# Kernel optimization log

Measured on AMD Instinct MI355X. Metric: run time of the kernel, lower is better.

Reference implementation:

```python
import jax, jax.numpy as jnp
import numpy as np

BETA = 1.0
GAMMA = 1.0
TAU = 1.0
EPS = 1e-8
RANK_CLAMP = 10  # torch.clamp(rank, max=10)


def _pearson(a, b):
    # a, b: [N, D]; pearson correlation along axis 1
    a = a - a.mean(axis=1, keepdims=True)
    b = b - b.mean(axis=1, keepdims=True)
    num = (a * b).sum(axis=1)
    den = jnp.linalg.norm(a, axis=1) * jnp.linalg.norm(b, axis=1) + EPS
    return num / den


def _filtered_ranks(y):
    # Vectorized equivalent of the per-row python loop: for each row, drop the
    # rank entry at the argmax position, yielding [B, C-1].
    B, C = y.shape
    j = jnp.argmax(y, axis=1)                       # [B]
    rank = jnp.minimum(jnp.argsort(y, axis=1), RANK_CLAMP)  # [B, C]
    base = jnp.arange(C - 1)[None, :]               # [1, C-1]
    idx = base + (base >= j[:, None]).astype(base.dtype)    # skip column j
    filt = jnp.take_along_axis(rank, idx, axis=1).astype(jnp.float32)
    return filt, j


def reference(z_s, z_t):
    y_s = jax.nn.softmax(z_s / TAU, axis=1)
    y_t = jax.nn.softmax(z_t / TAU, axis=1)

    # inter-class relation (spearman variant)
    fs, js = _filtered_ranks(y_s)
    ft, jt = _filtered_ranks(y_t)
    spearman = _pearson(fs, ft).mean()
    equal = (js == jt).astype(jnp.float32).mean()
    inter_loss = TAU ** 2 * (1.0 - (equal + spearman))

    # intra-class relation: pearson across batch per class
    intra_loss = TAU ** 2 * (1.0 - _pearson(y_s.T, y_t.T).mean())

    return BETA * inter_loss + GAMMA * intra_loss


def setup_inputs() -> dict:
    key = jax.random.key(0)
    k1, k2 = jax.random.split(key)
    B, C = 4096, 16000
    z_s = jax.random.normal(k1, (B, C), dtype=jnp.float32)
    z_t = jax.random.normal(k2, (B, C), dtype=jnp.float32)
    return {"z_s": z_s, "z_t": z_t}
```

## Files before the change

kernel.cpp:

```cpp
#include <hip/hip_runtime.h>
#include <math.h>

#define B_ROWS 4096
#define C_COLS 16000
#define NTH 10
static_assert((B_ROWS & (B_ROWS - 1)) == 0, "B pow2");

__device__ __forceinline__ void block_sum2(float& a, float& b) {
#pragma unroll
  for (int off = 32; off > 0; off >>= 1) {
    a += __shfl_down(a, off);
    b += __shfl_down(b, off);
  }
  __shared__ float sa[4], sb[4];
  const int w = threadIdx.x >> 6;
  if ((threadIdx.x & 63) == 0) { sa[w] = a; sb[w] = b; }
  __syncthreads();
  if (threadIdx.x == 0) {
    a = sa[0] + sa[1] + sa[2] + sa[3];
    b = sb[0] + sb[1] + sb[2] + sb[3];
  }
}

__global__ __launch_bounds__(256) void k_rowpass(
    const float* __restrict__ zs, const float* __restrict__ zt,
    float* __restrict__ rinv, int* __restrict__ jmax, int* __restrict__ pos)
{
  const int bid = blockIdx.x;
  const int m = bid >> 12;
  const int r = bid & (B_ROWS - 1);
  const float* __restrict__ z = (m ? zt : zs) + (size_t)r * C_COLS;

  float th[NTH];
#pragma unroll
  for (int i = 0; i < NTH; ++i) th[i] = z[i];

  int cnt[NTH];
#pragma unroll
  for (int i = 0; i < NTH; ++i) cnt[i] = 0;

  float vmax = -__builtin_inff();
  int vidx = 0;
  float sume = 0.f;

  const float4* __restrict__ z4 = (const float4*)z;
  for (int it = threadIdx.x; it < C_COLS / 4; it += 256) {
    const float4 v = z4[it];
    const int c = it * 4;
    const float xs[4] = {v.x, v.y, v.z, v.w};
#pragma unroll
    for (int u = 0; u < 4; ++u) {
      const float x = xs[u];
#pragma unroll
      for (int i = 0; i < NTH; ++i) cnt[i] += (x < th[i]) ? 1 : 0;
      if (x > vmax) { vmax = x; vidx = c + u; }
      sume += __expf(x);
    }
  }

#pragma unroll
  for (int off = 32; off > 0; off >>= 1) {
    sume += __shfl_down(sume, off);
#pragma unroll
    for (int i = 0; i < NTH; ++i) cnt[i] += __shfl_down(cnt[i], off);
    const float ov = __shfl_down(vmax, off);
    const int oi = __shfl_down(vidx, off);
    if (ov > vmax || (ov == vmax && oi < vidx)) { vmax = ov; vidx = oi; }
  }
  __shared__ float s_sum[4], s_max[4];
  __shared__ int s_idx[4], s_cnt[4][NTH];
  const int wave = threadIdx.x >> 6;
  if ((threadIdx.x & 63) == 0) {
    s_sum[wave] = sume; s_max[wave] = vmax; s_idx[wave] = vidx;
#pragma unroll
    for (int i = 0; i < NTH; ++i) s_cnt[wave][i] = cnt[i];
  }
  __syncthreads();
  if (threadIdx.x == 0) {
    float ts = 0.f, tm = s_max[0];
    int ti = s_idx[0];
    int tc[NTH];
#pragma unroll
    for (int i = 0; i < NTH; ++i) tc[i] = 0;
    for (int w = 0; w < 4; ++w) {
      ts += s_sum[w];
      if (s_max[w] > tm || (s_max[w] == tm && s_idx[w] < ti)) { tm = s_max[w]; ti = s_idx[w]; }
#pragma unroll
      for (int i = 0; i < NTH; ++i) tc[i] += s_cnt[w][i];
    }
    const int base = m * B_ROWS + r;
    rinv[base] = 1.f / ts;
    jmax[base] = ti;
#pragma unroll
    for (int i = 0; i < NTH; ++i) {
      int p = tc[i];
      for (int k = 0; k < i; ++k) p += (th[k] == th[i]) ? 1 : 0;
      pos[base * NTH + i] = p;
    }
  }
}

__global__ __launch_bounds__(256) void k_inter(
    const int* __restrict__ jmax, const int* __restrict__ pos,
    float* __restrict__ acc)
{
  const int r = blockIdx.x * 256 + threadIdx.x;
  float pear = 0.f, eq = 0.f;
  if (r < B_ROWS) {
    const int js = jmax[r];
    const int jt = jmax[B_ROWS + r];
    eq = (js == jt) ? 1.f : 0.f;
    int qs[NTH], qt[NTH];
    float vs[NTH], vt[NTH];
    int ns = 0, nt = 0;
    float sds = 0.f, sds2 = 0.f, sdt = 0.f, sdt2 = 0.f;
#pragma unroll
    for (int i = 0; i < NTH; ++i) {
      const float v = (float)(i - NTH);
      const int p = pos[r * NTH + i];
      if (p != js) {
        qs[ns] = p - (p > js ? 1 : 0);
        vs[ns] = v; ++ns;
        sds += v; sds2 += v * v;
      }
      const int p2 = pos[(B_ROWS + r) * NTH + i];
      if (p2 != jt) {
        qt[nt] = p2 - (p2 > jt ? 1 : 0);
        vt[nt] = v; ++nt;
        sdt += v; sdt2 += v * v;
      }
    }
    float sprod = 0.f;
    for (int a = 0; a < ns; ++a)
      for (int b = 0; b < nt; ++b)
        if (qs[a] == qt[b]) sprod += vs[a] * vt[b];
    const float Cm1 = (float)(C_COLS - 1);
    const float num  = sprod - sds * sdt / Cm1;
    const float vars = sds2 - sds * sds / Cm1;
    const float vart = sdt2 - sdt * sdt / Cm1;
    pear = num / (sqrtf(fmaxf(vars, 0.f)) * sqrtf(fmaxf(vart, 0.f)) + 1e-8f);
  }
  block_sum2(pear, eq);
  if (threadIdx.x == 0) {
    atomicAdd(&acc[0], pear);
    atomicAdd(&acc[1], eq);
  }
}

__global__ __launch_bounds__(256) void k_colpass(
    const float* __restrict__ zs, const float* __restrict__ zt,
    const float* __restrict__ rinv, float* __restrict__ colacc)
{
  const int c = blockIdx.x * 256 + threadIdx.x;
  const int r0 = blockIdx.y * 64;
  if (c >= C_COLS) return;
  float s1 = 0.f, s2 = 0.f, t1 = 0.f, t2 = 0.f, st = 0.f;
  size_t off = (size_t)r0 * C_COLS + (size_t)c;
#pragma unroll 4
  for (int k = 0; k < 64; ++k) {
    const float a = __expf(zs[off]) * rinv[r0 + k];
    const float b = __expf(zt[off]) * rinv[B_ROWS + r0 + k];
    s1 += a; s2 += a * a;
    t1 += b; t2 += b * b;
    st += a * b;
    off += C_COLS;
  }
  atomicAdd(&colacc[0 * C_COLS + c], s1);
  atomicAdd(&colacc[1 * C_COLS + c], t1);
  atomicAdd(&colacc[2 * C_COLS + c], s2);
  atomicAdd(&colacc[3 * C_COLS + c], t2);
  atomicAdd(&colacc[4 * C_COLS + c], st);
}

__global__ __launch_bounds__(256) void k_intra(
    const float* __restrict__ colacc, float* __restrict__ acc)
{
  const int c = blockIdx.x * 256 + threadIdx.x;
  float pear = 0.f, dummy = 0.f;
  if (c < C_COLS) {
    const float s1 = colacc[0 * C_COLS + c];
    const float t1 = colacc[1 * C_COLS + c];
    const float s2 = colacc[2 * C_COLS + c];
    const float t2 = colacc[3 * C_COLS + c];
    const float st = colacc[4 * C_COLS + c];
    const float Bf = (float)B_ROWS;
    const float num = st - s1 * t1 / Bf;
    const float vs = fmaxf(s2 - s1 * s1 / Bf, 0.f);
    const float vt = fmaxf(t2 - t1 * t1 / Bf, 0.f);
    pear = num / (sqrtf(vs) * sqrtf(vt) + 1e-8f);
  }
  block_sum2(pear, dummy);
  if (threadIdx.x == 0) atomicAdd(&acc[2], pear);
}

__global__ void k_final(const float* __restrict__ acc, float* __restrict__ out)
{
  if (threadIdx.x == 0) {
    const float spearman = acc[0] / (float)B_ROWS;
    const float eq = acc[1] / (float)B_ROWS;
    const float inter = 1.f - (eq + spearman);
    const float intra = 1.f - acc[2] / (float)C_COLS;
    out[0] = inter + intra;
  }
}

extern "C" void kernel_launch(void* const* d_in, const int* in_sizes, int n_in,
                              void* d_out, int out_size, void* d_ws, size_t ws_size,
                              hipStream_t stream) {
  const float* zs = (const float*)d_in[0];
  const float* zt = (const float*)d_in[1];
  float* out = (float*)d_out;
  float* ws = (float*)d_ws;

  float* rinv   = ws;
  int*   jmax   = (int*)(ws + 8192);
  int*   pos    = (int*)(ws + 16384);
  float* colacc = ws + 16384 + 81920;
  float* acc    = colacc + 5 * C_COLS;

  hipMemsetAsync(colacc, 0, (5 * C_COLS + 4) * sizeof(float), stream);

  k_rowpass<<<2 * B_ROWS, 256, 0, stream>>>(zs, zt, rinv, jmax, pos);
  k_inter<<<B_ROWS / 256, 256, 0, stream>>>(jmax, pos, acc);
  dim3 g3((C_COLS + 255) / 256, B_ROWS / 64);
  k_colpass<<<g3, 256, 0, stream>>>(zs, zt, rinv, colacc);
  k_intra<<<(C_COLS + 255) / 256, 256, 0, stream>>>(colacc, acc);
  k_final<<<1, 64, 0, stream>>>(acc, out);
}
```

Baseline: 619.8 us.

## Vectorize column pass, software-pipeline row pass, fold memset into row kernel

The row pass now prefetches the next float4 while processing the current one, keeps four independent max/sum accumulators, and reads thresholds through readfirstlane. The column pass loads float4 so each thread handles four columns, which gives wider loads and more work per thread. The inter kernel's variable-length compaction is replaced by fully unrolled masked loops, and the separate memset is folded into the row kernel. Together these aim to cut memory-bound load overhead, per-launch cost and loop-carried dependencies. In exchange, register pressure rises and the column grid has a quarter as many blocks.

```diff
diff --git a/kernel.cpp b/kernel.cpp
--- a/kernel.cpp
+++ b/kernel.cpp
@@ -4,7 +4,9 @@
 #define B_ROWS 4096
 #define C_COLS 16000
 #define NTH 10
+#define ROWF4 (C_COLS / 4)
 static_assert((B_ROWS & (B_ROWS - 1)) == 0, "B pow2");
+static_assert((C_COLS & 3) == 0, "C % 4");
 
 __device__ __forceinline__ void block_sum2(float& a, float& b) {
 #pragma unroll
@@ -24,38 +26,66 @@
 
 __global__ __launch_bounds__(256) void k_rowpass(
     const float* __restrict__ zs, const float* __restrict__ zt,
-    float* __restrict__ rinv, int* __restrict__ jmax, int* __restrict__ pos)
+    float* __restrict__ rinv, int* __restrict__ jmax, int* __restrict__ pos,
+    float* __restrict__ zero_region)
 {
   const int bid = blockIdx.x;
+
+  if (threadIdx.x < NTH) {
+    const int idx = bid * NTH + (int)threadIdx.x;
+    if (idx < 5 * C_COLS + 4) zero_region[idx] = 0.f;
+  }
+
   const int m = bid >> 12;
   const int r = bid & (B_ROWS - 1);
   const float* __restrict__ z = (m ? zt : zs) + (size_t)r * C_COLS;
 
   float th[NTH];
 #pragma unroll
-  for (int i = 0; i < NTH; ++i) th[i] = z[i];
+  for (int i = 0; i < NTH; ++i)
+    th[i] = __int_as_float(__builtin_amdgcn_readfirstlane(__float_as_int(z[i])));
 
   int cnt[NTH];
 #pragma unroll
   for (int i = 0; i < NTH; ++i) cnt[i] = 0;
 
-  float vmax = -__builtin_inff();
-  int vidx = 0;
-  float sume = 0.f;
+  float vmax[4]; int vit[4]; float se[4];
+#pragma unroll
+  for (int u = 0; u < 4; ++u) { vmax[u] = -__builtin_inff(); vit[u] = 0; se[u] = 0.f; }
 
   const float4* __restrict__ z4 = (const float4*)z;
-  for (int it = threadIdx.x; it < C_COLS / 4; it += 256) {
-    const float4 v = z4[it];
-    const int c = it * 4;
+
+  auto body = [&](const float4 v, const int itv) {
     const float xs[4] = {v.x, v.y, v.z, v.w};
 #pragma unroll
+    for (int i = 0; i < NTH; ++i)
+      cnt[i] += (int)(xs[0] < th[i]) + (int)(xs[1] < th[i]) +
+                (int)(xs[2] < th[i]) + (int)(xs[3] < th[i]);
+#pragma unroll
     for (int u = 0; u < 4; ++u) {
-      const float x = xs[u];
-#pragma unroll
-      for (int i = 0; i < NTH; ++i) cnt[i] += (x < th[i]) ? 1 : 0;
-      if (x > vmax) { vmax = x; vidx = c + u; }
-      sume += __expf(x);
-    }
+      se[u] += __expf(xs[u]);
+      if (xs[u] > vmax[u]) { vmax[u] = xs[u]; vit[u] = itv; }
+    }
+  };
+
+  const int iters = (ROWF4 >> 8) + ((threadIdx.x < (ROWF4 & 255)) ? 1 : 0);
+  int it = threadIdx.x;
+  float4 cur = z4[it];
+  for (int k = 1; k < iters; ++k) {
+    const float4 nxt = z4[it + 256];
+    body(cur, it);
+    it += 256;
+    cur = nxt;
+  }
+  body(cur, it);
+
+  float sume = (se[0] + se[1]) + (se[2] + se[3]);
+  float bmax = vmax[0];
+  int bidx = vit[0] * 4 + 0;
+#pragma unroll
+  for (int u = 1; u < 4; ++u) {
+    const int idx = vit[u] * 4 + u;
+    if (vmax[u] > bmax || (vmax[u] == bmax && idx < bidx)) { bmax = vmax[u]; bidx = idx; }
   }
 
 #pragma unroll
@@ -63,15 +93,15 @@
     sume += __shfl_down(sume, off);
 #pragma unroll
     for (int i = 0; i < NTH; ++i) cnt[i] += __shfl_down(cnt[i], off);
-    const float ov = __shfl_down(vmax, off);
-    const int oi = __shfl_down(vidx, off);
-    if (ov > vmax || (ov == vmax && oi < vidx)) { vmax = ov; vidx = oi; }
+    const float ov = __shfl_down(bmax, off);
+    const int oi = __shfl_down(bidx, off);
+    if (ov > bmax || (ov == bmax && oi < bidx)) { bmax = ov; bidx = oi; }
   }
   __shared__ float s_sum[4], s_max[4];
   __shared__ int s_idx[4], s_cnt[4][NTH];
   const int wave = threadIdx.x >> 6;
   if ((threadIdx.x & 63) == 0) {
-    s_sum[wave] = sume; s_max[wave] = vmax; s_idx[wave] = vidx;
+    s_sum[wave] = sume; s_max[wave] = bmax; s_idx[wave] = bidx;
 #pragma unroll
     for (int i = 0; i < NTH; ++i) s_cnt[wave][i] = cnt[i];
   }
@@ -110,30 +140,28 @@
     const int js = jmax[r];
     const int jt = jmax[B_ROWS + r];
     eq = (js == jt) ? 1.f : 0.f;
+    bool as[NTH], at[NTH];
     int qs[NTH], qt[NTH];
-    float vs[NTH], vt[NTH];
-    int ns = 0, nt = 0;
     float sds = 0.f, sds2 = 0.f, sdt = 0.f, sdt2 = 0.f;
 #pragma unroll
     for (int i = 0; i < NTH; ++i) {
       const float v = (float)(i - NTH);
       const int p = pos[r * NTH + i];
-      if (p != js) {
-        qs[ns] = p - (p > js ? 1 : 0);
-        vs[ns] = v; ++ns;
-        sds += v; sds2 += v * v;
-      }
+      as[i] = (p != js);
+      qs[i] = p - ((p > js) ? 1 : 0);
+      if (as[i]) { sds += v; sds2 += v * v; }
       const int p2 = pos[(B_ROWS + r) * NTH + i];
-      if (p2 != jt) {
-        qt[nt] = p2 - (p2 > jt ? 1 : 0);
-        vt[nt] = v; ++nt;
-        sdt += v; sdt2 += v * v;
-      }
+      at[i] = (p2 != jt);
+      qt[i] = p2 - ((p2 > jt) ? 1 : 0);
+      if (at[i]) { sdt += v; sdt2 += v * v; }
     }
     float sprod = 0.f;
-    for (int a = 0; a < ns; ++a)
-      for (int b = 0; b < nt; ++b)
-        if (qs[a] == qt[b]) sprod += vs[a] * vt[b];
+#pragma unroll
+    for (int a = 0; a < NTH; ++a)
+#pragma unroll
+      for (int b = 0; b < NTH; ++b)
+        if (as[a] && at[b] && (qs[a] == qt[b]))
+          sprod += (float)((a - NTH) * (b - NTH));
     const float Cm1 = (float)(C_COLS - 1);
     const float num  = sprod - sds * sdt / Cm1;
     const float vars = sds2 - sds * sds / Cm1;
@@ -147,29 +175,46 @@
   }
 }
 
+#define RPB 64
 __global__ __launch_bounds__(256) void k_colpass(
     const float* __restrict__ zs, const float* __restrict__ zt,
     const float* __restrict__ rinv, float* __restrict__ colacc)
 {
-  const int c = blockIdx.x * 256 + threadIdx.x;
-  const int r0 = blockIdx.y * 64;
-  if (c >= C_COLS) return;
-  float s1 = 0.f, s2 = 0.f, t1 = 0.f, t2 = 0.f, st = 0.f;
-  size_t off = (size_t)r0 * C_COLS + (size_t)c;
+  const int c4 = blockIdx.x * 256 + threadIdx.x;
+  if (c4 >= ROWF4) return;
+  const int r0 = blockIdx.y * RPB;
+  float s1[4] = {0,0,0,0}, s2[4] = {0,0,0,0}, t1[4] = {0,0,0,0},
+        t2[4] = {0,0,0,0}, st[4] = {0,0,0,0};
+  const float4* __restrict__ zs4 = (const float4*)zs;
+  const float4* __restrict__ zt4 = (const float4*)zt;
+  size_t off = (size_t)r0 * ROWF4 + (size_t)c4;
 #pragma unroll 4
-  for (int k = 0; k < 64; ++k) {
-    const float a = __expf(zs[off]) * rinv[r0 + k];
-    const float b = __expf(zt[off]) * rinv[B_ROWS + r0 + k];
-    s1 += a; s2 += a * a;
-    t1 += b; t2 += b * b;
-    st += a * b;
-    off += C_COLS;
-  }
-  atomicAdd(&colacc[0 * C_COLS + c], s1);
-  atomicAdd(&colacc[1 * C_COLS + c], t1);
-  atomicAdd(&colacc[2 * C_COLS + c], s2);
-  atomicAdd(&colacc[3 * C_COLS + c], t2);
-  atomicAdd(&colacc[4 * C_COLS + c], st);
+  for (int k = 0; k < RPB; ++k) {
+    const float ra = rinv[r0 + k];
+    const float rb = rinv[B_ROWS + r0 + k];
+    const float4 a4 = zs4[off];
+    const float4 b4 = zt4[off];
+    const float av[4] = {a4.x, a4.y, a4.z, a4.w};
+    const float bv[4] = {b4.x, b4.y, b4.z, b4.w};
+#pragma unroll
+    for (int u = 0; u < 4; ++u) {
+      const float a = __expf(av[u]) * ra;
+      const float b = __expf(bv[u]) * rb;
+      s1[u] += a; s2[u] += a * a;
+      t1[u] += b; t2[u] += b * b;
+      st[u] += a * b;
+    }
+    off += ROWF4;
+  }
+  const int c = c4 * 4;
+#pragma unroll
+  for (int u = 0; u < 4; ++u) {
+    atomicAdd(&colacc[0 * C_COLS + c + u], s1[u]);
+    atomicAdd(&colacc[1 * C_COLS + c + u], t1[u]);
+    atomicAdd(&colacc[2 * C_COLS + c + u], s2[u]);
+    atomicAdd(&colacc[3 * C_COLS + c + u], t2[u]);
+    atomicAdd(&colacc[4 * C_COLS + c + u], st[u]);
+  }
 }
 
 __global__ __launch_bounds__(256) void k_intra(
@@ -218,11 +263,9 @@
   float* colacc = ws + 16384 + 81920;
   float* acc    = colacc + 5 * C_COLS;
 
-  hipMemsetAsync(colacc, 0, (5 * C_COLS + 4) * sizeof(float), stream);
-
-  k_rowpass<<<2 * B_ROWS, 256, 0, stream>>>(zs, zt, rinv, jmax, pos);
+  k_rowpass<<<2 * B_ROWS, 256, 0, stream>>>(zs, zt, rinv, jmax, pos, colacc);
   k_inter<<<B_ROWS / 256, 256, 0, stream>>>(jmax, pos, acc);
-  dim3 g3((C_COLS + 255) / 256, B_ROWS / 64);
+  dim3 g3((ROWF4 + 255) / 256, B_ROWS / RPB);
   k_colpass<<<g3, 256, 0, stream>>>(zs, zt, rinv, colacc);
   k_intra<<<(C_COLS + 255) / 256, 256, 0, stream>>>(colacc, acc);
   k_final<<<1, 64, 0, stream>>>(acc, out);
```

Measured after the change: 662.3 us. +6.9%, slower.
